# Kernel tuning notes

Hardware: AMD Instinct MI355X
Metric: run time of the kernel (lower is better)

## Reference

```python
import jax, jax.numpy as jnp
import numpy as np

NUM_HEADS = 12


def setup_inputs() -> dict:
    key = jax.random.key(0)
    ks = jax.random.split(key, 6)
    C = 768
    hd = C // NUM_HEADS  # 64
    H = W = 32
    x = jax.random.normal(ks[0], (4, H, W, C), dtype=jnp.float32)
    # Linear weights stored as (in, out) so y = x @ W (+ b)
    Wqkv = jax.random.normal(ks[1], (C, 3 * C), dtype=jnp.float32) * 0.02
    Wproj = jax.random.normal(ks[2], (C, C), dtype=jnp.float32) * 0.02
    bproj = jax.random.normal(ks[3], (C,), dtype=jnp.float32) * 0.02
    rel_pos_h = jax.random.normal(ks[4], (2 * H - 1, hd), dtype=jnp.float32) * 0.02
    rel_pos_w = jax.random.normal(ks[5], (2 * W - 1, hd), dtype=jnp.float32) * 0.02
    return {"x": x, "Wqkv": Wqkv, "Wproj": Wproj, "bproj": bproj,
            "rel_pos_h": rel_pos_h, "rel_pos_w": rel_pos_w}


def _get_rel_pos(size: int, rel_pos: jnp.ndarray) -> jnp.ndarray:
    # q_size == k_size == size; table already has 2*size-1 entries -> no interpolation
    coords = jnp.arange(size)[:, None] - jnp.arange(size)[None, :] + (size - 1)
    return rel_pos[coords]  # (size, size, head_dim)


def reference(x, Wqkv, Wproj, bproj, rel_pos_h, rel_pos_w):
    B, H, W, C = x.shape
    hn = NUM_HEADS
    hd = C // hn
    scale = hd ** (-0.5)
    S = H * W

    qkv = x @ Wqkv                                   # (B,H,W,3C)
    qkv = qkv.reshape(B, S, 3, hn, hd)
    qkv = jnp.transpose(qkv, (2, 0, 3, 1, 4)).reshape(3, B * hn, S, hd)
    q, k, v = qkv[0], qkv[1], qkv[2]                 # each (B*hn, S, hd)

    # decomposed relative position bias
    Rh = _get_rel_pos(H, rel_pos_h)                  # (H,H,hd)
    Rw = _get_rel_pos(W, rel_pos_w)                  # (W,W,hd)
    r_q = q.reshape(B * hn, H, W, hd)
    rel_h = jnp.einsum('bhwc,hkc->bhwk', r_q, Rh)    # (B*hn,H,W,H)
    rel_w = jnp.einsum('bhwc,wkc->bhwk', r_q, Rw)    # (B*hn,H,W,W)
    bias = rel_h[..., :, None] + rel_w[..., None, :] # (B*hn,H,W,H,W)
    bias = bias.reshape(B * hn, S, S)

    scores = scale * jnp.einsum('bqc,bkc->bqk', q, k) + bias
    attn = jax.nn.softmax(scores, axis=-1)
    out = jnp.einsum('bqk,bkc->bqc', attn, v)        # (B*hn,S,hd)

    out = out.reshape(B, hn, H, W, hd)
    out = jnp.transpose(out, (0, 2, 3, 1, 4)).reshape(B, H, W, C)
    return out @ Wproj + bproj
```

## Files before the change

### kernel.cpp

```cpp
#include <hip/hip_runtime.h>
#include <stddef.h>

typedef __bf16 bf16x8 __attribute__((ext_vector_type(8)));
typedef __bf16 bf16x4 __attribute__((ext_vector_type(4)));
typedef _Float16 f16x4 __attribute__((ext_vector_type(4)));
typedef float  f32x4  __attribute__((ext_vector_type(4)));

#define MFMA16(a, b, c) __builtin_amdgcn_mfma_f32_16x16x32_bf16((a), (b), (c), 0, 0, 0)
#define MFMA16H(a, b, c) __builtin_amdgcn_mfma_f32_16x16x16f16((a), (b), (c), 0, 0, 0)
#define LOG2E 1.4426950408889634f

__device__ __forceinline__ void gload_lds16(const void* gsrc, void* ldst) {
    __builtin_amdgcn_global_load_lds(
        (__attribute__((address_space(1))) void*)gsrc,
        (__attribute__((address_space(3))) void*)ldst,
        16, 0, 0);
}

__global__ void prep_kernel(const float* __restrict__ x, __bf16* __restrict__ xbf,
                            const float* __restrict__ Wqkv, __bf16* __restrict__ WqkvT,
                            const float* __restrict__ Wproj, __bf16* __restrict__ WprojT) {
    __shared__ float tile[32][33];
    const int bx = blockIdx.x, tid = threadIdx.x;
    if (bx < 3072) {
        int i = bx * 256 + tid;
        float4 v = ((const float4*)x)[i];
        bf16x4 o = {(__bf16)v.x, (__bf16)v.y, (__bf16)v.z, (__bf16)v.w};
        ((bf16x4*)xbf)[i] = o;
        return;
    }
    const float* in; __bf16* out; int R, C, c0, r0;
    if (bx < 4800) { int bb = bx - 3072; in = Wqkv;  out = WqkvT;  R = 768; C = 2304;
                     c0 = (bb % 72) * 32; r0 = (bb / 72) * 32; }
    else           { int bb = bx - 4800; in = Wproj; out = WprojT; R = 768; C = 768;
                     c0 = (bb % 24) * 32; r0 = (bb / 24) * 32; }
    const int tx = tid & 31, ty = tid >> 5;
#pragma unroll
    for (int i = 0; i < 32; i += 8)
        tile[ty + i][tx] = in[(size_t)(r0 + ty + i) * C + c0 + tx];
    __syncthreads();
#pragma unroll
    for (int i = 0; i < 32; i += 8)
        out[(size_t)(c0 + ty + i) * R + r0 + tx] = (__bf16)tile[tx][ty + i];
}

__device__ __forceinline__ void gemm_core_bk64(
    const __bf16* __restrict__ A, const __bf16* __restrict__ Bt, int K,
    int m0, int n0, __bf16* aT, __bf16* bT, f32x4 acc[4][4]) {
    const int tid  = threadIdx.x;
    const int wid  = tid >> 6, lane = tid & 63;
    const int quad = lane >> 4, l16 = lane & 15;
    const int wm = (wid >> 1) * 64, wn = (wid & 1) * 64;
    const int r_in = lane >> 3;
    const int cswz = ((lane & 7) ^ r_in) * 8;
    const __bf16* gA = A  + (size_t)(m0 + wid * 8 + r_in) * K + cswz;
    const __bf16* gB = Bt + (size_t)(n0 + wid * 8 + r_in) * K + cswz;
    const int sA = (l16 & 7);
    for (int k0 = 0; k0 < K; k0 += 64) {
        __syncthreads();
#pragma unroll
        for (int j = 0; j < 4; j++) {
            gload_lds16(gA + (size_t)(j * 32) * K + k0, aT + (j * 32 + wid * 8) * 64);
            gload_lds16(gB + (size_t)(j * 32) * K + k0, bT + (j * 32 + wid * 8) * 64);
        }
        __syncthreads();
#pragma unroll
        for (int kh = 0; kh < 2; kh++) {
            bf16x8 af[4], bfr[4];
#pragma unroll
            for (int t = 0; t < 4; t++) {
                const int slot = ((kh * 4 + quad) ^ sA) << 3;
                af[t]  = *(const bf16x8*)(aT + (wm + t * 16 + l16) * 64 + slot);
                bfr[t] = *(const bf16x8*)(bT + (wn + t * 16 + l16) * 64 + slot);
            }
#pragma unroll
            for (int rt = 0; rt < 4; rt++)
#pragma unroll
                for (int ct = 0; ct < 4; ct++)
                    acc[rt][ct] = MFMA16(af[rt], bfr[ct], acc[rt][ct]);
        }
    }
}

__global__ __launch_bounds__(256, 3)
void gemm_qkv_kernel(const __bf16* __restrict__ A, const __bf16* __restrict__ Bt,
                     __bf16* __restrict__ qb, __bf16* __restrict__ kb,
                     _Float16* __restrict__ vtb) {
    __shared__ __bf16 aT[8192], bT[8192];
    f32x4 acc[4][4];
#pragma unroll
    for (int i = 0; i < 4; i++)
#pragma unroll
        for (int j = 0; j < 4; j++) { f32x4 z = {0.f, 0.f, 0.f, 0.f}; acc[i][j] = z; }
    const int m0 = blockIdx.x * 128, n0 = blockIdx.y * 128;
    gemm_core_bk64(A, Bt, 768, m0, n0, aT, bT, acc);
    const int tid = threadIdx.x, wid = tid >> 6, lane = tid & 63;
    const int quad = lane >> 4, l16 = lane & 15;
    const int wm = (wid >> 1) * 64, wn = (wid & 1) * 64;
#pragma unroll
    for (int rt = 0; rt < 4; rt++)
#pragma unroll
        for (int ct = 0; ct < 4; ct++) {
            const int ng = n0 + wn + ct * 16 + l16;
            const int which = ng / 768;
            const int rem = ng - which * 768;
            const int hh = rem >> 6, d = rem & 63;
#pragma unroll
            for (int r = 0; r < 4; r++) {
                const int mg = m0 + wm + rt * 16 + quad * 4 + r;
                const int b = mg >> 10, s = mg & 1023;
                const int bh = b * 12 + hh;
                if (which == 0)      qb[((size_t)bh * 1024 + s) * 64 + d] = (__bf16)acc[rt][ct][r];
                else if (which == 1) kb[((size_t)bh * 1024 + s) * 64 + d] = (__bf16)acc[rt][ct][r];
                else                 vtb[((size_t)bh * 64 + d) * 1024 + s] = (_Float16)acc[rt][ct][r];
            }
        }
}

__global__ __launch_bounds__(256, 3)
void gemm_proj_kernel(const __bf16* __restrict__ A, const __bf16* __restrict__ Bt,
                      const float* __restrict__ bias, float* __restrict__ out) {
    __shared__ __bf16 aT[8192], bT[8192];
    f32x4 acc[4][4];
#pragma unroll
    for (int i = 0; i < 4; i++)
#pragma unroll
        for (int j = 0; j < 4; j++) { f32x4 z = {0.f, 0.f, 0.f, 0.f}; acc[i][j] = z; }
    const int m0 = blockIdx.x * 128, n0 = blockIdx.y * 128;
    gemm_core_bk64(A, Bt, 768, m0, n0, aT, bT, acc);
    const int tid = threadIdx.x, wid = tid >> 6, lane = tid & 63;
    const int quad = lane >> 4, l16 = lane & 15;
    const int wm = (wid >> 1) * 64, wn = (wid & 1) * 64;
#pragma unroll
    for (int rt = 0; rt < 4; rt++)
#pragma unroll
        for (int ct = 0; ct < 4; ct++) {
            const int ng = n0 + wn + ct * 16 + l16;
            const float bb = bias[ng];
#pragma unroll
            for (int r = 0; r < 4; r++) {
                const int mg = m0 + wm + rt * 16 + quad * 4 + r;
                out[(size_t)mg * 768 + ng] = acc[rt][ct][r] + bb;
            }
        }
}

__global__ __launch_bounds__(128, 2)
void attn_kernel(const __bf16* __restrict__ q, const __bf16* __restrict__ kk,
                 const _Float16* __restrict__ vt, const float* __restrict__ rph,
                 const float* __restrict__ rpw, __bf16* __restrict__ aout) {
    __shared__ __bf16   kbuf2[2][4096];
    __shared__ _Float16 vbuf2[2][4096];
    __shared__ float    relh[64][33];
    const int tid = threadIdx.x, wid = tid >> 6, lane = tid & 63;
    const int quad = lane >> 4, l16 = lane & 15;
    const int bh = blockIdx.x, qt = blockIdx.y;
    const int b = bh / 12, hh = bh - b * 12;
    const int q0 = qt * 64;
    const int w0 = wid * 32;
    const int h = qt * 2 + wid;

    bf16x8 aq[2][2];
#pragma unroll
    for (int rt = 0; rt < 2; rt++) {
        const __bf16* qp = q + ((size_t)bh * 1024 + q0 + w0 + rt * 16 + l16) * 64;
        aq[rt][0] = *(const bf16x8*)(qp + quad * 8);
        aq[rt][1] = *(const bf16x8*)(qp + 32 + quad * 8);
    }

    float* Dw = ((float*)kbuf2) + wid * 2048;
#pragma unroll
    for (int ct = 0; ct < 4; ct++) {
        int j = ct * 16 + l16; if (j > 62) j = 62;
        const float* tb = rpw + (size_t)j * 64;
        float4 t0 = *(const float4*)(tb + quad * 8);
        float4 t1 = *(const float4*)(tb + quad * 8 + 4);
        float4 t2 = *(const float4*)(tb + 32 + quad * 8);
        float4 t3 = *(const float4*)(tb + 32 + quad * 8 + 4);
        bf16x8 b0 = {(__bf16)t0.x, (__bf16)t0.y, (__bf16)t0.z, (__bf16)t0.w,
                     (__bf16)t1.x, (__bf16)t1.y, (__bf16)t1.z, (__bf16)t1.w};
        bf16x8 b1 = {(__bf16)t2.x, (__bf16)t2.y, (__bf16)t2.z, (__bf16)t2.w,
                     (__bf16)t3.x, (__bf16)t3.y, (__bf16)t3.z, (__bf16)t3.w};
#pragma unroll
        for (int rt = 0; rt < 2; rt++) {
            f32x4 z = {0.f, 0.f, 0.f, 0.f};
            z = MFMA16(aq[rt][0], b0, z);
            z = MFMA16(aq[rt][1], b1, z);
#pragma unroll
            for (int i = 0; i < 4; i++)
                Dw[(rt * 16 + quad * 4 + i) * 64 + ct * 16 + l16] = z[i];
        }
    }
#pragma unroll
    for (int ct = 0; ct < 2; ct++) {
        const int tr = h - (ct * 16 + l16) + 31;
        const float* tb = rph + (size_t)tr * 64;
        float4 t0 = *(const float4*)(tb + quad * 8);
        float4 t1 = *(const float4*)(tb + quad * 8 + 4);
        float4 t2 = *(const float4*)(tb + 32 + quad * 8);
        float4 t3 = *(const float4*)(tb + 32 + quad * 8 + 4);
        bf16x8 b0 = {(__bf16)t0.x, (__bf16)t0.y, (__bf16)t0.z, (__bf16)t0.w,
                     (__bf16)t1.x, (__bf16)t1.y, (__bf16)t1.z, (__bf16)t1.w};
        bf16x8 b1 = {(__bf16)t2.x, (__bf16)t2.y, (__bf16)t2.z, (__bf16)t2.w,
                     (__bf16)t3.x, (__bf16)t3.y, (__bf16)t3.z, (__bf16)t3.w};
#pragma unroll
        for (int rt = 0; rt < 2; rt++) {
            f32x4 z = {0.f, 0.f, 0.f, 0.f};
            z = MFMA16(aq[rt][0], b0, z);
            z = MFMA16(aq[rt][1], b1, z);
#pragma unroll
            for (int i = 0; i < 4; i++)
                relh[w0 + rt * 16 + quad * 4 + i][ct * 16 + l16] = z[i] * LOG2E;
        }
    }
    float bw[2][2][4];
#pragma unroll
    for (int rt = 0; rt < 2; rt++) {
        const int rl = rt * 16 + l16;
#pragma unroll
        for (int hf = 0; hf < 2; hf++)
#pragma unroll
            for (int r = 0; r < 4; r++)
                bw[rt][hf][r] = LOG2E * Dw[rl * 64 + rl + 31 - hf * 16 - quad * 4 - r];
    }
    __syncthreads();

    float l_run[2] = {0.f, 0.f};
    f32x4 o_acc[2][4];
#pragma unroll
    for (int rt = 0; rt < 2; rt++)
#pragma unroll
        for (int t = 0; t < 4; t++) { f32x4 z = {0.f, 0.f, 0.f, 0.f}; o_acc[rt][t] = z; }

    const __bf16*   kg0 = kk + (size_t)bh * 65536;
    const _Float16* vg0 = vt + (size_t)bh * 65536;
    const int cbase = wid * 4;
    const int srow = lane >> 3;
    const int scol = ((lane & 7) ^ srow) * 8;
    const int swz0 = ((quad ^ (l16 & 7)) << 3);
    const int swz1 = (((quad | 4) ^ (l16 & 7)) << 3);
    const int l7 = l16 & 7, qhi = quad >> 1, qlo = (quad & 1) * 4;
    const float SC = 0.125f * LOG2E;

    auto stage = [&](int buf, int kt) {
        const __bf16*   kg = kg0 + kt * 4096;
        const _Float16* vg = vg0 + kt * 64;
        __bf16*   kb_ = &kbuf2[buf][0];
        _Float16* vb_ = &vbuf2[buf][0];
#pragma unroll
        for (int j = 0; j < 4; j++) {
            const int c = cbase + j;
            gload_lds16(kg + (c * 8 + srow) * 64 + scol, kb_ + c * 512);
            gload_lds16(vg + (size_t)(c * 8 + srow) * 1024 + scol, vb_ + c * 512);
        }
    };

    stage(0, 0);
    for (int kt = 0; kt < 16; kt++) {
        const int cur = kt & 1;
        __syncthreads();
        if (kt < 15) stage(1 - cur, kt + 1);
        const __bf16*   kbuf = &kbuf2[cur][0];
        const _Float16* vbuf = &vbuf2[cur][0];

        bf16x8 bk[4][2];
#pragma unroll
        for (int ct = 0; ct < 4; ct++) {
            const int key = ct * 16 + l16;
            bk[ct][0] = *(const bf16x8*)(kbuf + key * 64 + swz0);
            bk[ct][1] = *(const bf16x8*)(kbuf + key * 64 + swz1);
        }

        f32x4 sacc[2][4];
#pragma unroll
        for (int rt = 0; rt < 2; rt++)
#pragma unroll
            for (int ct = 0; ct < 4; ct++) {
                f32x4 z = {0.f, 0.f, 0.f, 0.f};
                z = MFMA16(bk[ct][0], aq[rt][0], z);
                z = MFMA16(bk[ct][1], aq[rt][1], z);
                sacc[rt][ct] = z;
            }

        f16x4 pf[2][4];
#pragma unroll
        for (int rt = 0; rt < 2; rt++) {
            const float bh0 = relh[w0 + rt * 16 + l16][kt * 2];
            const float bh1 = relh[w0 + rt * 16 + l16][kt * 2 + 1];
#pragma unroll
            for (int ct = 0; ct < 4; ct++) {
                const float bhc = (ct < 2) ? bh0 : bh1;
#pragma unroll
                for (int r = 0; r < 4; r++) {
                    float sv = fmaf(sacc[rt][ct][r], SC, bhc + bw[rt][ct & 1][r]);
                    float p = exp2f(sv);
                    l_run[rt] += p;
                    pf[rt][ct][r] = (_Float16)p;
                }
            }
        }

#pragma unroll
        for (int dt = 0; dt < 4; dt++) {
            const int vrow = (dt * 16 + l16) * 64;
#pragma unroll
            for (int ct = 0; ct < 4; ct++) {
                const int slot = (ct * 2 + qhi) ^ l7;
                f16x4 vf = *(const f16x4*)(vbuf + vrow + slot * 8 + qlo);
                o_acc[0][dt] = MFMA16H(vf, pf[0][ct], o_acc[0][dt]);
                o_acc[1][dt] = MFMA16H(vf, pf[1][ct], o_acc[1][dt]);
            }
        }
    }

#pragma unroll
    for (int rt = 0; rt < 2; rt++) {
        float s = l_run[rt];
        s += __shfl_xor(s, 16);
        s += __shfl_xor(s, 32);
        const float inv = 1.f / s;
        const int srow_o = q0 + w0 + rt * 16 + l16;
#pragma unroll
        for (int dt = 0; dt < 4; dt++) {
            bf16x4 ov = {(__bf16)(o_acc[rt][dt][0] * inv), (__bf16)(o_acc[rt][dt][1] * inv),
                         (__bf16)(o_acc[rt][dt][2] * inv), (__bf16)(o_acc[rt][dt][3] * inv)};
            *(bf16x4*)&aout[((size_t)b * 1024 + srow_o) * 768 + hh * 64 + dt * 16 + quad * 4] = ov;
        }
    }
}

extern "C" void kernel_launch(void* const* d_in, const int* in_sizes, int n_in,
                              void* d_out, int out_size, void* d_ws, size_t ws_size,
                              hipStream_t stream) {
    const float* x     = (const float*)d_in[0];
    const float* Wqkv  = (const float*)d_in[1];
    const float* Wproj = (const float*)d_in[2];
    const float* bproj = (const float*)d_in[3];
    const float* rph   = (const float*)d_in[4];
    const float* rpw   = (const float*)d_in[5];
    float* out = (float*)d_out;
    char* ws = (char*)d_ws;

    __bf16*   xbf    = (__bf16*)(ws);
    __bf16*   WqkvT  = (__bf16*)(ws + 6291456);
    __bf16*   WprojT = (__bf16*)(ws + 9830400);
    __bf16*   qb     = (__bf16*)(ws + 11010048);
    __bf16*   kb     = (__bf16*)(ws + 17301504);
    _Float16* vtb    = (_Float16*)(ws + 23592960);
    __bf16*   aob    = (__bf16*)(ws + 29884416);

    prep_kernel<<<dim3(5376), dim3(256), 0, stream>>>(x, xbf, Wqkv, WqkvT, Wproj, WprojT);
    gemm_qkv_kernel<<<dim3(32, 18), dim3(256), 0, stream>>>(xbf, WqkvT, qb, kb, vtb);
    attn_kernel<<<dim3(48, 16), dim3(128), 0, stream>>>(qb, kb, vtb, rph, rpw, aob);
    gemm_proj_kernel<<<dim3(32, 6), dim3(256), 0, stream>>>(aob, WprojT, bproj, out);
}
```

Baseline: 157.3 us.

## Enlarge attention query tile to 128 rows with four waves sharing K/V staging

The attention kernel now runs 256-thread blocks covering 128 query rows, so each staged K/V tile is shared by four waves instead of two and each wave issues half as many async loads. The relative-height bias table is stored as fp16 in a single shared buffer to keep LDS use near 40KB, and the launch bound targets three blocks per CU. The QKV GEMM epilogue also writes the transposed V output as packed 4-element f16 vectors instead of scalar stores. Risks include fp16 precision loss on the bias and fewer blocks in the attention grid.

Result: faster. 152.7 us (-3.0%).

```diff
diff --git a/kernel.cpp b/kernel.cpp
--- a/kernel.cpp
+++ b/kernel.cpp
@@ -4,6 +4,7 @@
 typedef __bf16 bf16x8 __attribute__((ext_vector_type(8)));
 typedef __bf16 bf16x4 __attribute__((ext_vector_type(4)));
 typedef _Float16 f16x4 __attribute__((ext_vector_type(4)));
+typedef _Float16 f16x2 __attribute__((ext_vector_type(2)));
 typedef float  f32x4  __attribute__((ext_vector_type(4)));
 
 #define MFMA16(a, b, c) __builtin_amdgcn_mfma_f32_16x16x32_bf16((a), (b), (c), 0, 0, 0)
@@ -105,14 +106,18 @@
             const int which = ng / 768;
             const int rem = ng - which * 768;
             const int hh = rem >> 6, d = rem & 63;
-#pragma unroll
-            for (int r = 0; r < 4; r++) {
-                const int mg = m0 + wm + rt * 16 + quad * 4 + r;
-                const int b = mg >> 10, s = mg & 1023;
-                const int bh = b * 12 + hh;
-                if (which == 0)      qb[((size_t)bh * 1024 + s) * 64 + d] = (__bf16)acc[rt][ct][r];
-                else if (which == 1) kb[((size_t)bh * 1024 + s) * 64 + d] = (__bf16)acc[rt][ct][r];
-                else                 vtb[((size_t)bh * 64 + d) * 1024 + s] = (_Float16)acc[rt][ct][r];
+            const int mg0 = m0 + wm + rt * 16 + quad * 4;
+            const int b0 = mg0 >> 10, s0 = mg0 & 1023;
+            const int bh = b0 * 12 + hh;
+            if (which == 2) {
+                f16x4 vv = {(_Float16)acc[rt][ct][0], (_Float16)acc[rt][ct][1],
+                            (_Float16)acc[rt][ct][2], (_Float16)acc[rt][ct][3]};
+                *(f16x4*)&vtb[((size_t)bh * 64 + d) * 1024 + s0] = vv;
+            } else {
+                __bf16* dst = (which == 0) ? qb : kb;
+#pragma unroll
+                for (int r = 0; r < 4; r++)
+                    dst[((size_t)bh * 1024 + s0 + r) * 64 + d] = (__bf16)acc[rt][ct][r];
             }
         }
 }
@@ -145,20 +150,21 @@
         }
 }
 
-__global__ __launch_bounds__(128, 2)
+__global__ __launch_bounds__(256, 3)
 void attn_kernel(const __bf16* __restrict__ q, const __bf16* __restrict__ kk,
                  const _Float16* __restrict__ vt, const float* __restrict__ rph,
                  const float* __restrict__ rpw, __bf16* __restrict__ aout) {
-    __shared__ __bf16   kbuf2[2][4096];
-    __shared__ _Float16 vbuf2[2][4096];
-    __shared__ float    relh[64][33];
+    __shared__ __attribute__((aligned(16))) unsigned char smem[41472];
+    __bf16*   kbufs = (__bf16*)smem;
+    _Float16* vbufs = (_Float16*)(smem + 16384);
+    _Float16 (*relh)[34] = (_Float16(*)[34])(smem + 32768);
     const int tid = threadIdx.x, wid = tid >> 6, lane = tid & 63;
     const int quad = lane >> 4, l16 = lane & 15;
     const int bh = blockIdx.x, qt = blockIdx.y;
     const int b = bh / 12, hh = bh - b * 12;
-    const int q0 = qt * 64;
+    const int q0 = qt * 128;
     const int w0 = wid * 32;
-    const int h = qt * 2 + wid;
+    const int h = qt * 4 + wid;
 
     bf16x8 aq[2][2];
 #pragma unroll
@@ -168,7 +174,7 @@
         aq[rt][1] = *(const bf16x8*)(qp + 32 + quad * 8);
     }
 
-    float* Dw = ((float*)kbuf2) + wid * 2048;
+    float* Dw = ((float*)smem) + wid * 2048;
 #pragma unroll
     for (int ct = 0; ct < 4; ct++) {
         int j = ct * 16 + l16; if (j > 62) j = 62;
@@ -210,7 +216,7 @@
             z = MFMA16(aq[rt][1], b1, z);
 #pragma unroll
             for (int i = 0; i < 4; i++)
-                relh[w0 + rt * 16 + quad * 4 + i][ct * 16 + l16] = z[i] * LOG2E;
+                relh[w0 + rt * 16 + quad * 4 + i][ct * 16 + l16] = (_Float16)(z[i] * LOG2E);
         }
     }
     float bw[2][2][4];
@@ -234,7 +240,7 @@
 
     const __bf16*   kg0 = kk + (size_t)bh * 65536;
     const _Float16* vg0 = vt + (size_t)bh * 65536;
-    const int cbase = wid * 4;
+    const int cbase = wid * 2;
     const int srow = lane >> 3;
     const int scol = ((lane & 7) ^ srow) * 8;
     const int swz0 = ((quad ^ (l16 & 7)) << 3);
@@ -245,10 +251,10 @@
     auto stage = [&](int buf, int kt) {
         const __bf16*   kg = kg0 + kt * 4096;
         const _Float16* vg = vg0 + kt * 64;
-        __bf16*   kb_ = &kbuf2[buf][0];
-        _Float16* vb_ = &vbuf2[buf][0];
-#pragma unroll
-        for (int j = 0; j < 4; j++) {
+        __bf16*   kb_ = kbufs + buf * 4096;
+        _Float16* vb_ = vbufs + buf * 4096;
+#pragma unroll
+        for (int j = 0; j < 2; j++) {
             const int c = cbase + j;
             gload_lds16(kg + (c * 8 + srow) * 64 + scol, kb_ + c * 512);
             gload_lds16(vg + (size_t)(c * 8 + srow) * 1024 + scol, vb_ + c * 512);
@@ -260,8 +266,8 @@
         const int cur = kt & 1;
         __syncthreads();
         if (kt < 15) stage(1 - cur, kt + 1);
-        const __bf16*   kbuf = &kbuf2[cur][0];
-        const _Float16* vbuf = &vbuf2[cur][0];
+        const __bf16*   kbuf = kbufs + cur * 4096;
+        const _Float16* vbuf = vbufs + cur * 4096;
 
         bf16x8 bk[4][2];
 #pragma unroll
@@ -285,8 +291,8 @@
         f16x4 pf[2][4];
 #pragma unroll
         for (int rt = 0; rt < 2; rt++) {
-            const float bh0 = relh[w0 + rt * 16 + l16][kt * 2];
-            const float bh1 = relh[w0 + rt * 16 + l16][kt * 2 + 1];
+            f16x2 bhp = *(const f16x2*)&relh[w0 + rt * 16 + l16][kt * 2];
+            const float bh0 = (float)bhp[0], bh1 = (float)bhp[1];
 #pragma unroll
             for (int ct = 0; ct < 4; ct++) {
                 const float bhc = (ct < 2) ? bh0 : bh1;
@@ -351,6 +357,6 @@
 
     prep_kernel<<<dim3(5376), dim3(256), 0, stream>>>(x, xbf, Wqkv, WqkvT, Wproj, WprojT);
     gemm_qkv_kernel<<<dim3(32, 18), dim3(256), 0, stream>>>(xbf, WqkvT, qb, kb, vtb);
-    attn_kernel<<<dim3(48, 16), dim3(128), 0, stream>>>(qb, kb, vtb, rph, rpw, aob);
+    attn_kernel<<<dim3(48, 8), dim3(256), 0, stream>>>(qb, kb, vtb, rph, rpw, aob);
     gemm_proj_kernel<<<dim3(32, 6), dim3(256), 0, stream>>>(aob, WprojT, bproj, out);
 }
```
